# Optimization experiments

Hardware: AMD Instinct MI355X
Metric: run time of the kernel (lower is better)

The kernel has to match this reference:

```python
import jax, jax.numpy as jnp
import numpy as np

D_MODEL = 1024
N_HEAD = 16
D_HEAD = 64


def setup_inputs() -> dict:
    key = jax.random.key(0)
    k1, k2, k3 = jax.random.split(key, 3)
    B, T = 2, 2048
    x = jax.random.normal(k1, (B, T, D_MODEL), dtype=jnp.float32)
    # Linear weights (scaled like typical init to keep softmax numerics sane)
    w_attn = jax.random.normal(k2, (D_MODEL, 3 * D_MODEL), dtype=jnp.float32) * (1.0 / np.sqrt(D_MODEL))
    w_proj = jax.random.normal(k3, (D_MODEL, D_MODEL), dtype=jnp.float32) * (1.0 / np.sqrt(D_MODEL))
    return {"x": x, "w_attn": w_attn, "w_proj": w_proj}


def reference(x, w_attn, w_proj):
    B, T, C = x.shape
    # c_attn: fused qkv projection (use_bias=False)
    qkv = jnp.einsum('btc,cf->btf', x, w_attn)  # [B, T, 3C]
    q, k, v = jnp.split(qkv, 3, axis=-1)
    q = q.reshape(B, T, N_HEAD, D_HEAD)
    k = k.reshape(B, T, N_HEAD, D_HEAD)
    v = v.reshape(B, T, N_HEAD, D_HEAD)
    # scaled QK^T with causal mask (cache=None training path)
    att = jnp.einsum('bqhd,bkhd->bhqk', q, k) * (1.0 / jnp.sqrt(jnp.float32(D_HEAD)))
    causal = jnp.tril(jnp.ones((T, T), dtype=bool))  # [T, T]
    att = jnp.where(causal[None, None, :, :], att, -jnp.inf)
    att = jax.nn.softmax(att, axis=-1)
    # dropout is a no-op (deterministic / p=0)
    y = jnp.einsum('bhqk,bkhd->bqhd', att, v).reshape(B, T, C)
    y = jnp.einsum('btc,cd->btd', y, w_proj)
    return y
```

## Files before the change

### kernel.cpp

```cpp
#include <hip/hip_runtime.h>
#include <hip/hip_bf16.h>


typedef __attribute__((ext_vector_type(8))) __bf16 bf16x8;
typedef __attribute__((ext_vector_type(4))) float  floatx4;
typedef __attribute__((ext_vector_type(4))) float  fvec4;
typedef __attribute__((ext_vector_type(4))) short  short4v;

#define MFMA16(a, b, c) __builtin_amdgcn_mfma_f32_16x16x32_bf16(a, b, c, 0, 0, 0)

using as1v = const __attribute__((address_space(1))) void;
using as3v = __attribute__((address_space(3))) void;
__device__ __forceinline__ void async16(const void* g, void* l) {
  __builtin_amdgcn_global_load_lds((as1v*)g, (as3v*)l, 16, 0, 0);
}

__device__ inline void store_out(float* p, float v) { *p = v; }
__device__ inline void store_out(__hip_bfloat16* p, float v) { *p = __float2bfloat16(v); }

__global__ __launch_bounds__(256) void prep_kernel(const float* __restrict__ x,
                                                   const float* __restrict__ w_attn,
                                                   const float* __restrict__ w_proj,
                                                   __hip_bfloat16* __restrict__ xb,
                                                   __hip_bfloat16* __restrict__ wat,
                                                   __hip_bfloat16* __restrict__ wpt) {
  const int bid = blockIdx.x, tid = threadIdx.x;
  if (bid < 4096) {
    const int i = (bid * 256 + tid) * 4;
    fvec4 v = *(const fvec4*)(x + i);
    union { short4v s; __hip_bfloat16 h[4]; } u;
#pragma unroll
    for (int j = 0; j < 4; ++j) u.h[j] = __float2bfloat16(v[j]);
    *(short4v*)((short*)xb + i) = u.s;
    return;
  }
  __shared__ __align__(16) __hip_bfloat16 tile[64 * 64];
  const float* in;
  __hip_bfloat16* out;
  int cols, bx, by;
  if (bid < 4864) {
    const int b2 = bid - 4096;
    in = w_attn; out = wat; cols = 3072; bx = b2 % 48; by = b2 / 48;
  } else {
    const int b2 = bid - 4864;
    in = w_proj; out = wpt; cols = 1024; bx = b2 % 16; by = b2 / 16;
  }
  const int c0 = bx * 64, r0 = by * 64;
#pragma unroll
  for (int it = 0; it < 2; ++it) {
    const int c = it * 256 + tid;
    const int row = c >> 3, cg = c & 7;
    const float* src = in + (long)(r0 + row) * cols + c0 + cg * 8;
    fvec4 v0 = *(const fvec4*)src;
    fvec4 v1 = *(const fvec4*)(src + 4);
    union { bf16x8 v; __hip_bfloat16 h[8]; } u;
#pragma unroll
    for (int j = 0; j < 4; ++j) { u.h[j] = __float2bfloat16(v0[j]); u.h[4 + j] = __float2bfloat16(v1[j]); }
    *(bf16x8*)(tile + row * 64 + (cg ^ ((row >> 3) & 7)) * 8) = u.v;
  }
  __syncthreads();
#pragma unroll
  for (int it = 0; it < 2; ++it) {
    const int c = it * 256 + tid;
    const int dr = c >> 3, tg = c & 7;
    union { bf16x8 v; __hip_bfloat16 e[8]; } u;
    const int pg = (dr >> 3) ^ tg;
#pragma unroll
    for (int j = 0; j < 8; ++j)
      u.e[j] = tile[(tg * 8 + j) * 64 + pg * 8 + (dr & 7)];
    *(bf16x8*)(out + (long)(c0 + dr) * 1024 + r0 + tg * 8) = u.v;
  }
}

__global__ __launch_bounds__(256) void gemm_qkv_kernel(const __hip_bfloat16* __restrict__ A,
                                                       const __hip_bfloat16* __restrict__ Bt,
                                                       __hip_bfloat16* __restrict__ qk,
                                                       __hip_bfloat16* __restrict__ vt,
                                                       float qscale) {
  const int K = 1024;
  __shared__ __align__(16) __hip_bfloat16 As[2][128 * 32];
  __shared__ __align__(16) __hip_bfloat16 Bs[2][128 * 32];
  const int tid = threadIdx.x;
  const int lane = tid & 63, wv = tid >> 6;
  const int l15 = lane & 15, quad = lane >> 4;
  const int wm = wv >> 1, wn = wv & 1;
  const long m0 = (long)blockIdx.y * 128, n0 = (long)blockIdx.x * 128;
  floatx4 acc[4][4] = {};
  const int nk = K >> 5;

  auto issue = [&](int kt, int p) {
    const int k0 = kt << 5;
#pragma unroll
    for (int it = 0; it < 2; ++it) {
      const int c = it * 256 + tid;
      const int row = c >> 2;
      const int lcg = (c & 3) ^ ((row >> 1) & 3);
      async16(A + (m0 + row) * K + k0 + lcg * 8, (char*)&As[p][0] + c * 16);
      async16(Bt + (n0 + row) * K + k0 + lcg * 8, (char*)&Bs[p][0] + c * 16);
    }
  };

  issue(0, 0);
  for (int kt = 0; kt < nk; ++kt) {
    const int p = kt & 1;
    __syncthreads();
    if (kt + 1 < nk) issue(kt + 1, p ^ 1);
    bf16x8 af[4], bfr[4];
#pragma unroll
    for (int t = 0; t < 4; ++t) {
      const int ar = wm * 64 + t * 16 + l15;
      const int br = wn * 64 + t * 16 + l15;
      af[t]  = *(const bf16x8*)(&As[p][ar * 32 + (quad ^ ((ar >> 1) & 3)) * 8]);
      bfr[t] = *(const bf16x8*)(&Bs[p][br * 32 + (quad ^ ((br >> 1) & 3)) * 8]);
    }
#pragma unroll
    for (int mt = 0; mt < 4; ++mt)
#pragma unroll
      for (int nt = 0; nt < 4; ++nt)
        acc[mt][nt] = MFMA16(af[mt], bfr[nt], acc[mt][nt]);
  }

#pragma unroll
  for (int nt = 0; nt < 4; ++nt) {
    const int colb = (int)n0 + wn * 64 + nt * 16;
    if (colb >= 2048) {
      const int hh = (colb - 2048) >> 6;
      const int d  = (colb & 63) + l15;
#pragma unroll
      for (int mt = 0; mt < 4; ++mt) {
        const long row = m0 + wm * 64 + mt * 16 + quad * 4;
        const long b   = row >> 11;
        const long t0  = row & 2047;
        union { short4v s; __hip_bfloat16 h[4]; } uy;
#pragma unroll
        for (int r = 0; r < 4; ++r) uy.h[r] = __float2bfloat16(acc[mt][nt][r]);
        *(short4v*)(vt + ((b * 16 + hh) * 64 + d) * 2048 + t0) = uy.s;
      }
    } else {
      const float sc = (colb < 1024) ? qscale : 1.0f;
      const long col = colb + l15;
#pragma unroll
      for (int mt = 0; mt < 4; ++mt)
#pragma unroll
        for (int r = 0; r < 4; ++r) {
          const long row = m0 + wm * 64 + mt * 16 + quad * 4 + r;
          qk[row * 2048 + col] = __float2bfloat16(acc[mt][nt][r] * sc);
        }
    }
  }
}

template <typename OutT>
__global__ __launch_bounds__(256) void gemm_bt64_kernel(const __hip_bfloat16* __restrict__ A,
                                                        const __hip_bfloat16* __restrict__ Bt,
                                                        OutT* __restrict__ C,
                                                        int M, int N, int K) {
  __shared__ __align__(16) __hip_bfloat16 As[2][128 * 32];
  __shared__ __align__(16) __hip_bfloat16 Bs[2][64 * 32];
  const int tid = threadIdx.x;
  const int lane = tid & 63, wv = tid >> 6;
  const int l15 = lane & 15, quad = lane >> 4;
  const int wm = wv >> 1, wn = wv & 1;
  const long m0 = (long)blockIdx.y * 128, n0 = (long)blockIdx.x * 64;
  floatx4 acc[4][2] = {};
  const int nk = K >> 5;

  auto issue = [&](int kt, int p) {
    const int k0 = kt << 5;
#pragma unroll
    for (int it = 0; it < 2; ++it) {
      const int c = it * 256 + tid;
      const int row = c >> 2;
      const int lcg = (c & 3) ^ ((row >> 1) & 3);
      async16(A + (m0 + row) * K + k0 + lcg * 8, (char*)&As[p][0] + c * 16);
    }
    {
      const int c = tid;
      const int row = c >> 2;
      const int lcg = (c & 3) ^ ((row >> 1) & 3);
      async16(Bt + (n0 + row) * K + k0 + lcg * 8, (char*)&Bs[p][0] + c * 16);
    }
  };

  issue(0, 0);
  for (int kt = 0; kt < nk; ++kt) {
    const int p = kt & 1;
    __syncthreads();
    if (kt + 1 < nk) issue(kt + 1, p ^ 1);
    bf16x8 af[4], bfr[2];
#pragma unroll
    for (int t = 0; t < 4; ++t) {
      const int ar = wm * 64 + t * 16 + l15;
      af[t] = *(const bf16x8*)(&As[p][ar * 32 + (quad ^ ((ar >> 1) & 3)) * 8]);
    }
#pragma unroll
    for (int t = 0; t < 2; ++t) {
      const int br = wn * 32 + t * 16 + l15;
      bfr[t] = *(const bf16x8*)(&Bs[p][br * 32 + (quad ^ ((br >> 1) & 3)) * 8]);
    }
#pragma unroll
    for (int mt = 0; mt < 4; ++mt)
#pragma unroll
      for (int nt = 0; nt < 2; ++nt)
        acc[mt][nt] = MFMA16(af[mt], bfr[nt], acc[mt][nt]);
  }
#pragma unroll
  for (int mt = 0; mt < 4; ++mt)
#pragma unroll
    for (int nt = 0; nt < 2; ++nt)
#pragma unroll
      for (int r = 0; r < 4; ++r) {
        const long row = m0 + wm * 64 + mt * 16 + quad * 4 + r;
        const long col = n0 + wn * 32 + nt * 16 + l15;
        store_out(C + row * N + col, acc[mt][nt][r]);
      }
}

__global__ __launch_bounds__(256) void attn_kernel(const __hip_bfloat16* __restrict__ qk,
                                                   const __hip_bfloat16* __restrict__ vtg,
                                                   __hip_bfloat16* __restrict__ y) {
  __shared__ __align__(16) __hip_bfloat16 Ks[2][64 * 64];
  __shared__ __align__(16) __hip_bfloat16 Vt[2][64 * 64];
  __shared__ __align__(16) __hip_bfloat16 Pb[4][16 * 64];
  const int tid = threadIdx.x;
  const int lane = tid & 63, wv = tid >> 6;
  const int l15 = lane & 15, quad = lane >> 4;
  const int pt = blockIdx.x, h = blockIdx.y, b = blockIdx.z;
  const int qtA = pt, qtB = 31 - pt;
  const int q0A = qtA * 64, q0B = qtB * 64;
  const long bh = (long)b * 16 + h;
  const long RS = 2048;

  auto issue = [&](int kt, int p) {
    const int kb = kt * 64;
#pragma unroll
    for (int it = 0; it < 2; ++it) {
      const int c = it * 256 + tid;
      const int row = c >> 3;
      const int cg = (c & 7) ^ (row & 7);
      async16(qk + ((long)b * 2048 + kb + row) * RS + 1024 + h * 64 + cg * 8,
              (char*)&Ks[p][0] + c * 16);
      async16(vtg + (bh * 64 + row) * 2048 + kb + cg * 8, (char*)&Vt[p][0] + c * 16);
    }
  };

  bf16x8 bqA0, bqA1, bqB0, bqB1;
  {
    const __hip_bfloat16* qpA = qk + ((long)b * 2048 + q0A + wv * 16 + l15) * RS + h * 64 + quad * 8;
    bqA0 = *(const bf16x8*)qpA;
    bqA1 = *(const bf16x8*)(qpA + 32);
    const __hip_bfloat16* qpB = qk + ((long)b * 2048 + q0B + wv * 16 + l15) * RS + h * 64 + quad * 8;
    bqB0 = *(const bf16x8*)qpB;
    bqB1 = *(const bf16x8*)(qpB + 32);
  }
  union { bf16x8 v; __hip_bfloat16 e[8]; } uo;
#pragma unroll
  for (int j = 0; j < 8; ++j) uo.e[j] = __float2bfloat16(1.0f);
  const bf16x8 ones = uo.v;

  floatx4 oA[4] = {}, oB[4] = {}, o4A = {}, o4B = {};
  __hip_bfloat16* Pw = &Pb[wv][0];
  const int m7 = l15 & 7;

  issue(0, 0);
  for (int kt = 0; kt <= qtB; ++kt) {
    const int p = kt & 1;
    const int kb = kt * 64;
    const bool actA = (kt <= qtA);
    __syncthreads();
    if (kt < qtB) issue(kt + 1, p ^ 1);

    bf16x8 kf[4][2], vf[4][2];
#pragma unroll
    for (int nt = 0; nt < 4; ++nt) {
      const int row = nt * 16 + l15;
      const int s0 = (quad ^ (row & 7)) * 8, s1 = ((quad + 4) ^ (row & 7)) * 8;
      kf[nt][0] = *(const bf16x8*)(&Ks[p][row * 64 + s0]);
      kf[nt][1] = *(const bf16x8*)(&Ks[p][row * 64 + s1]);
      vf[nt][0] = *(const bf16x8*)(&Vt[p][row * 64 + s0]);
      vf[nt][1] = *(const bf16x8*)(&Vt[p][row * 64 + s1]);
    }

    auto tile = [&](const bf16x8& bq0, const bf16x8& bq1, floatx4* o, floatx4& o4,
                    bool diag, int q0X) {
      floatx4 st[4] = {};
#pragma unroll
      for (int nt = 0; nt < 4; ++nt) {
        st[nt] = MFMA16(kf[nt][0], bq0, st[nt]);
        st[nt] = MFMA16(kf[nt][1], bq1, st[nt]);
      }
      const int qg = q0X + wv * 16 + l15;
#pragma unroll
      for (int nt = 0; nt < 4; ++nt) {
        union { short4v s; __hip_bfloat16 h[4]; } up;
#pragma unroll
        for (int r = 0; r < 4; ++r) {
          float pv = exp2f(st[nt][r]);
          if (diag && (kb + nt * 16 + quad * 4 + r > qg)) pv = 0.f;
          up.h[r] = __float2bfloat16(pv);
        }
        const int chunk = (nt * 2 + (quad >> 1)) ^ m7;
        *(short4v*)(Pw + l15 * 64 + chunk * 8 + (quad & 1) * 4) = up.s;
      }
      const bf16x8 pb0 = *(const bf16x8*)(Pw + l15 * 64 + (quad ^ m7) * 8);
      const bf16x8 pb1 = *(const bf16x8*)(Pw + l15 * 64 + ((quad + 4) ^ m7) * 8);
#pragma unroll
      for (int mt = 0; mt < 4; ++mt) {
        o[mt] = MFMA16(vf[mt][0], pb0, o[mt]);
        o[mt] = MFMA16(vf[mt][1], pb1, o[mt]);
      }
      o4 = MFMA16(ones, pb0, o4);
      o4 = MFMA16(ones, pb1, o4);
    };

    tile(bqB0, bqB1, oB, o4B, kt == qtB, q0B);
    if (actA) tile(bqA0, bqA1, oA, o4A, kt == qtA, q0A);
  }

  auto epi = [&](floatx4* o, floatx4& o4, int q0X) {
    const float inv = 1.0f / o4[0];
    const long t = (long)b * 2048 + q0X + wv * 16 + l15;
#pragma unroll
    for (int mt = 0; mt < 4; ++mt) {
      union { short4v s; __hip_bfloat16 h[4]; } uy;
#pragma unroll
      for (int r = 0; r < 4; ++r) uy.h[r] = __float2bfloat16(o[mt][r] * inv);
      *(short4v*)(y + t * 1024 + h * 64 + mt * 16 + quad * 4) = uy.s;
    }
  };
  epi(oA, o4A, q0A);
  epi(oB, o4B, q0B);
}

extern "C" void kernel_launch(void* const* d_in, const int* in_sizes, int n_in,
                              void* d_out, int out_size, void* d_ws, size_t ws_size,
                              hipStream_t stream) {
  const float* x      = (const float*)d_in[0];
  const float* w_attn = (const float*)d_in[1];
  const float* w_proj = (const float*)d_in[2];
  float* out = (float*)d_out;
  char* ws = (char*)d_ws;
  __hip_bfloat16* xb  = (__hip_bfloat16*)(ws);
  __hip_bfloat16* wat = (__hip_bfloat16*)(ws + 8388608);
  __hip_bfloat16* qk  = (__hip_bfloat16*)(ws + 16777216);
  __hip_bfloat16* wpt = (__hip_bfloat16*)(ws + 33554432);
  __hip_bfloat16* vtg = (__hip_bfloat16*)(ws + 35651584);
  __hip_bfloat16* yb  = wat;
  const float SC = 0.18033688011112042f;

  prep_kernel<<<5120, 256, 0, stream>>>(x, w_attn, w_proj, xb, wat, wpt);
  gemm_qkv_kernel<<<dim3(24, 32), 256, 0, stream>>>(xb, wat, qk, vtg, SC);
  attn_kernel<<<dim3(16, 16, 2), 256, 0, stream>>>(qk, vtg, yb);
  gemm_bt64_kernel<float><<<dim3(16, 32), 256, 0, stream>>>(yb, wpt, out, 4096, 1024, 1024);
}
```

Measured before the change: 182.0 us.

## Stage V-transpose epilogue through LDS and interleave paired attention tiles

The QKV GEMM's V-transpose epilogue now writes the accumulator tile into the reused shared-memory buffer with a swizzle. It then emits full 16-byte coalesced stores to the transposed V layout, replacing scattered 8-byte stores. The attention kernel splits the P scratch into separate buffers for the two query tiles and interleaves their QK MFMAs, softmax and PV MFMAs. This exposes more independent MFMA work per iteration to hide latency, at the cost of more registers and doubled P shared memory.

```diff
diff --git a/kernel.cpp b/kernel.cpp
--- a/kernel.cpp
+++ b/kernel.cpp
@@ -78,8 +78,7 @@
                                                        __hip_bfloat16* __restrict__ vt,
                                                        float qscale) {
   const int K = 1024;
-  __shared__ __align__(16) __hip_bfloat16 As[2][128 * 32];
-  __shared__ __align__(16) __hip_bfloat16 Bs[2][128 * 32];
+  __shared__ __align__(16) __hip_bfloat16 smem[16384];
   const int tid = threadIdx.x;
   const int lane = tid & 63, wv = tid >> 6;
   const int l15 = lane & 15, quad = lane >> 4;
@@ -95,8 +94,8 @@
       const int c = it * 256 + tid;
       const int row = c >> 2;
       const int lcg = (c & 3) ^ ((row >> 1) & 3);
-      async16(A + (m0 + row) * K + k0 + lcg * 8, (char*)&As[p][0] + c * 16);
-      async16(Bt + (n0 + row) * K + k0 + lcg * 8, (char*)&Bs[p][0] + c * 16);
+      async16(A + (m0 + row) * K + k0 + lcg * 8, (char*)(smem + p * 4096) + c * 16);
+      async16(Bt + (n0 + row) * K + k0 + lcg * 8, (char*)(smem + 8192 + p * 4096) + c * 16);
     }
   };
 
@@ -105,13 +104,15 @@
     const int p = kt & 1;
     __syncthreads();
     if (kt + 1 < nk) issue(kt + 1, p ^ 1);
+    const __hip_bfloat16* As = smem + p * 4096;
+    const __hip_bfloat16* Bs = smem + 8192 + p * 4096;
     bf16x8 af[4], bfr[4];
 #pragma unroll
     for (int t = 0; t < 4; ++t) {
       const int ar = wm * 64 + t * 16 + l15;
       const int br = wn * 64 + t * 16 + l15;
-      af[t]  = *(const bf16x8*)(&As[p][ar * 32 + (quad ^ ((ar >> 1) & 3)) * 8]);
-      bfr[t] = *(const bf16x8*)(&Bs[p][br * 32 + (quad ^ ((br >> 1) & 3)) * 8]);
+      af[t]  = *(const bf16x8*)(As + ar * 32 + (quad ^ ((ar >> 1) & 3)) * 8);
+      bfr[t] = *(const bf16x8*)(Bs + br * 32 + (quad ^ ((br >> 1) & 3)) * 8);
     }
 #pragma unroll
     for (int mt = 0; mt < 4; ++mt)
@@ -120,23 +121,38 @@
         acc[mt][nt] = MFMA16(af[mt], bfr[nt], acc[mt][nt]);
   }
 
-#pragma unroll
-  for (int nt = 0; nt < 4; ++nt) {
-    const int colb = (int)n0 + wn * 64 + nt * 16;
-    if (colb >= 2048) {
-      const int hh = (colb - 2048) >> 6;
-      const int d  = (colb & 63) + l15;
-#pragma unroll
-      for (int mt = 0; mt < 4; ++mt) {
-        const long row = m0 + wm * 64 + mt * 16 + quad * 4;
-        const long b   = row >> 11;
-        const long t0  = row & 2047;
+  if (n0 >= 2048) {
+    __syncthreads();
+#pragma unroll
+    for (int mt = 0; mt < 4; ++mt)
+#pragma unroll
+      for (int nt = 0; nt < 4; ++nt) {
+        const int mb = wm * 64 + mt * 16 + quad * 4;
+        const int n  = wn * 64 + nt * 16 + l15;
+        const int cchunk = mb >> 4;
+        const int phys = cchunk ^ (n & 7);
         union { short4v s; __hip_bfloat16 h[4]; } uy;
 #pragma unroll
         for (int r = 0; r < 4; ++r) uy.h[r] = __float2bfloat16(acc[mt][nt][r]);
-        *(short4v*)(vt + ((b * 16 + hh) * 64 + d) * 2048 + t0) = uy.s;
-      }
-    } else {
+        *(short4v*)(smem + n * 128 + phys * 16 + (mb & 15)) = uy.s;
+      }
+    __syncthreads();
+    const int h0 = ((int)n0 - 2048) >> 6;
+    const long b  = m0 >> 11;
+    const long t0 = m0 & 2047;
+#pragma unroll
+    for (int j = 0; j < 8; ++j) {
+      const int idx = j * 256 + tid;
+      const int n = idx >> 4, lo = idx & 15;
+      const int phys = (lo >> 1) ^ (n & 7);
+      bf16x8 v = *(const bf16x8*)(smem + n * 128 + phys * 16 + (lo & 1) * 8);
+      const int h = h0 + (n >> 6), d = n & 63;
+      *(bf16x8*)(vt + ((b * 16 + h) * 64 + d) * 2048 + t0 + lo * 8) = v;
+    }
+  } else {
+#pragma unroll
+    for (int nt = 0; nt < 4; ++nt) {
+      const int colb = (int)n0 + wn * 64 + nt * 16;
       const float sc = (colb < 1024) ? qscale : 1.0f;
       const long col = colb + l15;
 #pragma unroll
@@ -221,7 +237,7 @@
                                                    __hip_bfloat16* __restrict__ y) {
   __shared__ __align__(16) __hip_bfloat16 Ks[2][64 * 64];
   __shared__ __align__(16) __hip_bfloat16 Vt[2][64 * 64];
-  __shared__ __align__(16) __hip_bfloat16 Pb[4][16 * 64];
+  __shared__ __align__(16) __hip_bfloat16 Pb[8192];
   const int tid = threadIdx.x;
   const int lane = tid & 63, wv = tid >> 6;
   const int l15 = lane & 15, quad = lane >> 4;
@@ -259,8 +275,10 @@
   const bf16x8 ones = uo.v;
 
   floatx4 oA[4] = {}, oB[4] = {}, o4A = {}, o4B = {};
-  __hip_bfloat16* Pw = &Pb[wv][0];
+  __hip_bfloat16* PwB = Pb + wv * 1024;
+  __hip_bfloat16* PwA = Pb + 4096 + wv * 1024;
   const int m7 = l15 & 7;
+  const int qg_off = wv * 16 + l15;
 
   issue(0, 0);
   for (int kt = 0; kt <= qtB; ++kt) {
@@ -281,40 +299,73 @@
       vf[nt][1] = *(const bf16x8*)(&Vt[p][row * 64 + s1]);
     }
 
-    auto tile = [&](const bf16x8& bq0, const bf16x8& bq1, floatx4* o, floatx4& o4,
-                    bool diag, int q0X) {
-      floatx4 st[4] = {};
+    floatx4 stB[4] = {}, stA[4] = {};
+#pragma unroll
+    for (int nt = 0; nt < 4; ++nt) {
+      stB[nt] = MFMA16(kf[nt][0], bqB0, stB[nt]);
+      stB[nt] = MFMA16(kf[nt][1], bqB1, stB[nt]);
+    }
+    if (actA) {
 #pragma unroll
       for (int nt = 0; nt < 4; ++nt) {
-        st[nt] = MFMA16(kf[nt][0], bq0, st[nt]);
-        st[nt] = MFMA16(kf[nt][1], bq1, st[nt]);
-      }
-      const int qg = q0X + wv * 16 + l15;
+        stA[nt] = MFMA16(kf[nt][0], bqA0, stA[nt]);
+        stA[nt] = MFMA16(kf[nt][1], bqA1, stA[nt]);
+      }
+    }
+
+    {
+      const int qg = q0B + qg_off;
+      const bool diag = (kt == qtB);
 #pragma unroll
       for (int nt = 0; nt < 4; ++nt) {
         union { short4v s; __hip_bfloat16 h[4]; } up;
 #pragma unroll
         for (int r = 0; r < 4; ++r) {
-          float pv = exp2f(st[nt][r]);
+          float pv = exp2f(stB[nt][r]);
           if (diag && (kb + nt * 16 + quad * 4 + r > qg)) pv = 0.f;
           up.h[r] = __float2bfloat16(pv);
         }
         const int chunk = (nt * 2 + (quad >> 1)) ^ m7;
-        *(short4v*)(Pw + l15 * 64 + chunk * 8 + (quad & 1) * 4) = up.s;
-      }
-      const bf16x8 pb0 = *(const bf16x8*)(Pw + l15 * 64 + (quad ^ m7) * 8);
-      const bf16x8 pb1 = *(const bf16x8*)(Pw + l15 * 64 + ((quad + 4) ^ m7) * 8);
+        *(short4v*)(PwB + l15 * 64 + chunk * 8 + (quad & 1) * 4) = up.s;
+      }
+    }
+    if (actA) {
+      const int qg = q0A + qg_off;
+      const bool diag = (kt == qtA);
+#pragma unroll
+      for (int nt = 0; nt < 4; ++nt) {
+        union { short4v s; __hip_bfloat16 h[4]; } up;
+#pragma unroll
+        for (int r = 0; r < 4; ++r) {
+          float pv = exp2f(stA[nt][r]);
+          if (diag && (kb + nt * 16 + quad * 4 + r > qg)) pv = 0.f;
+          up.h[r] = __float2bfloat16(pv);
+        }
+        const int chunk = (nt * 2 + (quad >> 1)) ^ m7;
+        *(short4v*)(PwA + l15 * 64 + chunk * 8 + (quad & 1) * 4) = up.s;
+      }
+    }
+
+    const bf16x8 pbB0 = *(const bf16x8*)(PwB + l15 * 64 + (quad ^ m7) * 8);
+    const bf16x8 pbB1 = *(const bf16x8*)(PwB + l15 * 64 + ((quad + 4) ^ m7) * 8);
+#pragma unroll
+    for (int mt = 0; mt < 4; ++mt) {
+      oB[mt] = MFMA16(vf[mt][0], pbB0, oB[mt]);
+      oB[mt] = MFMA16(vf[mt][1], pbB1, oB[mt]);
+    }
+    o4B = MFMA16(ones, pbB0, o4B);
+    o4B = MFMA16(ones, pbB1, o4B);
+    if (actA) {
+      const bf16x8 pbA0 = *(const bf16x8*)(PwA + l15 * 64 + (quad ^ m7) * 8);
+      const bf16x8 pbA1 = *(const bf16x8*)(PwA + l15 * 64 + ((quad + 4) ^ m7) * 8);
 #pragma unroll
       for (int mt = 0; mt < 4; ++mt) {
-        o[mt] = MFMA16(vf[mt][0], pb0, o[mt]);
-        o[mt] = MFMA16(vf[mt][1], pb1, o[mt]);
-      }
-      o4 = MFMA16(ones, pb0, o4);
-      o4 = MFMA16(ones, pb1, o4);
-    };
-
-    tile(bqB0, bqB1, oB, o4B, kt == qtB, q0B);
-    if (actA) tile(bqA0, bqA1, oA, o4A, kt == qtA, q0A);
+        oA[mt] = MFMA16(vf[mt][0], pbA0, oA[mt]);
+        oA[mt] = MFMA16(vf[mt][1], pbA1, oA[mt]);
+      }
+      o4A = MFMA16(ones, pbA0, o4A);
+      o4A = MFMA16(ones, pbA1, o4A);
+    }
   }
 
   auto epi = [&](floatx4* o, floatx4& o4, int q0X) {
```

New measurement: 187.1 us. 1.03x slower.

## Stage V-transpose epilogue through LDS, split P buffers, remap attention grid

Applied to the files above, without the earlier changes.

The QKV GEMM epilogue for V-columns now writes the accumulator tile into shared memory with a swizzle, then emits coalesced 16-byte stores to the transposed V layout instead of scattered 8-byte stores. The attention kernel gets separate P staging buffers for the A and B query tiles, which removes the write-after-read hazard between the two tile calls. It also uses a 1D grid remapped so that consecutive blocks share the same query-tile pair across heads, which may improve cache locality. The costs are an extra LDS round trip and two barriers in the epilogue, plus doubled P buffer LDS in attention.

```diff
diff --git a/kernel.cpp b/kernel.cpp
--- a/kernel.cpp
+++ b/kernel.cpp
@@ -78,8 +78,7 @@
                                                        __hip_bfloat16* __restrict__ vt,
                                                        float qscale) {
   const int K = 1024;
-  __shared__ __align__(16) __hip_bfloat16 As[2][128 * 32];
-  __shared__ __align__(16) __hip_bfloat16 Bs[2][128 * 32];
+  __shared__ __align__(16) __hip_bfloat16 smem[16384];
   const int tid = threadIdx.x;
   const int lane = tid & 63, wv = tid >> 6;
   const int l15 = lane & 15, quad = lane >> 4;
@@ -95,8 +94,8 @@
       const int c = it * 256 + tid;
       const int row = c >> 2;
       const int lcg = (c & 3) ^ ((row >> 1) & 3);
-      async16(A + (m0 + row) * K + k0 + lcg * 8, (char*)&As[p][0] + c * 16);
-      async16(Bt + (n0 + row) * K + k0 + lcg * 8, (char*)&Bs[p][0] + c * 16);
+      async16(A + (m0 + row) * K + k0 + lcg * 8, (char*)(smem + p * 4096) + c * 16);
+      async16(Bt + (n0 + row) * K + k0 + lcg * 8, (char*)(smem + 8192 + p * 4096) + c * 16);
     }
   };
 
@@ -105,13 +104,15 @@
     const int p = kt & 1;
     __syncthreads();
     if (kt + 1 < nk) issue(kt + 1, p ^ 1);
+    const __hip_bfloat16* As = smem + p * 4096;
+    const __hip_bfloat16* Bs = smem + 8192 + p * 4096;
     bf16x8 af[4], bfr[4];
 #pragma unroll
     for (int t = 0; t < 4; ++t) {
       const int ar = wm * 64 + t * 16 + l15;
       const int br = wn * 64 + t * 16 + l15;
-      af[t]  = *(const bf16x8*)(&As[p][ar * 32 + (quad ^ ((ar >> 1) & 3)) * 8]);
-      bfr[t] = *(const bf16x8*)(&Bs[p][br * 32 + (quad ^ ((br >> 1) & 3)) * 8]);
+      af[t]  = *(const bf16x8*)(As + ar * 32 + (quad ^ ((ar >> 1) & 3)) * 8);
+      bfr[t] = *(const bf16x8*)(Bs + br * 32 + (quad ^ ((br >> 1) & 3)) * 8);
     }
 #pragma unroll
     for (int mt = 0; mt < 4; ++mt)
@@ -120,23 +121,37 @@
         acc[mt][nt] = MFMA16(af[mt], bfr[nt], acc[mt][nt]);
   }
 
-#pragma unroll
-  for (int nt = 0; nt < 4; ++nt) {
-    const int colb = (int)n0 + wn * 64 + nt * 16;
-    if (colb >= 2048) {
-      const int hh = (colb - 2048) >> 6;
-      const int d  = (colb & 63) + l15;
-#pragma unroll
-      for (int mt = 0; mt < 4; ++mt) {
-        const long row = m0 + wm * 64 + mt * 16 + quad * 4;
-        const long b   = row >> 11;
-        const long t0  = row & 2047;
+  if (n0 >= 2048) {
+    __syncthreads();
+#pragma unroll
+    for (int mt = 0; mt < 4; ++mt)
+#pragma unroll
+      for (int nt = 0; nt < 4; ++nt) {
+        const int mb = wm * 64 + mt * 16 + quad * 4;
+        const int n  = wn * 64 + nt * 16 + l15;
+        const int phys = (mb >> 4) ^ (n & 7);
         union { short4v s; __hip_bfloat16 h[4]; } uy;
 #pragma unroll
         for (int r = 0; r < 4; ++r) uy.h[r] = __float2bfloat16(acc[mt][nt][r]);
-        *(short4v*)(vt + ((b * 16 + hh) * 64 + d) * 2048 + t0) = uy.s;
-      }
-    } else {
+        *(short4v*)(smem + n * 128 + phys * 16 + (mb & 15)) = uy.s;
+      }
+    __syncthreads();
+    const int h0 = ((int)n0 - 2048) >> 6;
+    const long b  = m0 >> 11;
+    const long t0 = m0 & 2047;
+#pragma unroll
+    for (int j = 0; j < 8; ++j) {
+      const int idx = j * 256 + tid;
+      const int n = idx >> 4, lo = idx & 15;
+      const int phys = (lo >> 1) ^ (n & 7);
+      bf16x8 v = *(const bf16x8*)(smem + n * 128 + phys * 16 + (lo & 1) * 8);
+      const int h = h0 + (n >> 6), d = n & 63;
+      *(bf16x8*)(vt + ((b * 16 + h) * 64 + d) * 2048 + t0 + lo * 8) = v;
+    }
+  } else {
+#pragma unroll
+    for (int nt = 0; nt < 4; ++nt) {
+      const int colb = (int)n0 + wn * 64 + nt * 16;
       const float sc = (colb < 1024) ? qscale : 1.0f;
       const long col = colb + l15;
 #pragma unroll
@@ -221,11 +236,14 @@
                                                    __hip_bfloat16* __restrict__ y) {
   __shared__ __align__(16) __hip_bfloat16 Ks[2][64 * 64];
   __shared__ __align__(16) __hip_bfloat16 Vt[2][64 * 64];
-  __shared__ __align__(16) __hip_bfloat16 Pb[4][16 * 64];
+  __shared__ __align__(16) __hip_bfloat16 Pb[8192];
   const int tid = threadIdx.x;
   const int lane = tid & 63, wv = tid >> 6;
   const int l15 = lane & 15, quad = lane >> 4;
-  const int pt = blockIdx.x, h = blockIdx.y, b = blockIdx.z;
+  const int bid = blockIdx.x;
+  const int pt = (bid >> 3) & 15;
+  const int hb = (bid >> 7) * 8 + (bid & 7);
+  const int h = hb & 15, b = hb >> 4;
   const int qtA = pt, qtB = 31 - pt;
   const int q0A = qtA * 64, q0B = qtB * 64;
   const long bh = (long)b * 16 + h;
@@ -259,7 +277,8 @@
   const bf16x8 ones = uo.v;
 
   floatx4 oA[4] = {}, oB[4] = {}, o4A = {}, o4B = {};
-  __hip_bfloat16* Pw = &Pb[wv][0];
+  __hip_bfloat16* PwB = Pb + wv * 1024;
+  __hip_bfloat16* PwA = Pb + 4096 + wv * 1024;
   const int m7 = l15 & 7;
 
   issue(0, 0);
@@ -282,7 +301,7 @@
     }
 
     auto tile = [&](const bf16x8& bq0, const bf16x8& bq1, floatx4* o, floatx4& o4,
-                    bool diag, int q0X) {
+                    __hip_bfloat16* Pw, bool diag, int q0X) {
       floatx4 st[4] = {};
 #pragma unroll
       for (int nt = 0; nt < 4; ++nt) {
@@ -313,8 +332,8 @@
       o4 = MFMA16(ones, pb1, o4);
     };
 
-    tile(bqB0, bqB1, oB, o4B, kt == qtB, q0B);
-    if (actA) tile(bqA0, bqA1, oA, o4A, kt == qtA, q0A);
+    tile(bqB0, bqB1, oB, o4B, PwB, kt == qtB, q0B);
+    if (actA) tile(bqA0, bqA1, oA, o4A, PwA, kt == qtA, q0A);
   }
 
   auto epi = [&](floatx4* o, floatx4& o4, int q0X) {
@@ -350,6 +369,6 @@
 
   prep_kernel<<<5120, 256, 0, stream>>>(x, w_attn, w_proj, xb, wat, wpt);
   gemm_qkv_kernel<<<dim3(24, 32), 256, 0, stream>>>(xb, wat, qk, vtg, SC);
-  attn_kernel<<<dim3(16, 16, 2), 256, 0, stream>>>(qk, vtg, yb);
+  attn_kernel<<<512, 256, 0, stream>>>(qk, vtg, yb);
   gemm_bt64_kernel<float><<<dim3(16, 32), 256, 0, stream>>>(yb, wpt, out, 4096, 1024, 1024);
 }
```

Measured after the change: 184.5 us. No clear change (+1.4%).

## Transpose MFMA operands for vectorized epilogue stores, remap attention grid, split P buffers

Applied to the files above, without the earlier changes.

In the QK part of the QKV GEMM and in the output projection GEMM, the MFMA operand order is swapped so each lane holds four consecutive columns. This lets the epilogue write 8-byte bf16 or 16-byte float vectors instead of scalar strided stores, cutting store instruction count and improving coalescing. The attention kernel moves to a 1D grid whose block index maps so that eight heads share each pair index, which may improve CU/XCD placement and L2 locality. It also gives the A and B tiles separate P scratch buffers so the two tile computations do not serialize on shared LDS, at the cost of doubling that buffer.

```diff
diff --git a/kernel.cpp b/kernel.cpp
--- a/kernel.cpp
+++ b/kernel.cpp
@@ -14,9 +14,6 @@
 __device__ __forceinline__ void async16(const void* g, void* l) {
   __builtin_amdgcn_global_load_lds((as1v*)g, (as3v*)l, 16, 0, 0);
 }
-
-__device__ inline void store_out(float* p, float v) { *p = v; }
-__device__ inline void store_out(__hip_bfloat16* p, float v) { *p = __float2bfloat16(v); }
 
 __global__ __launch_bounds__(256) void prep_kernel(const float* __restrict__ x,
                                                    const float* __restrict__ w_attn,
@@ -87,6 +84,7 @@
   const long m0 = (long)blockIdx.y * 128, n0 = (long)blockIdx.x * 128;
   floatx4 acc[4][4] = {};
   const int nk = K >> 5;
+  const bool isV = (n0 >= 2048);
 
   auto issue = [&](int kt, int p) {
     const int k0 = kt << 5;
@@ -113,17 +111,25 @@
       af[t]  = *(const bf16x8*)(&As[p][ar * 32 + (quad ^ ((ar >> 1) & 3)) * 8]);
       bfr[t] = *(const bf16x8*)(&Bs[p][br * 32 + (quad ^ ((br >> 1) & 3)) * 8]);
     }
-#pragma unroll
-    for (int mt = 0; mt < 4; ++mt)
-#pragma unroll
-      for (int nt = 0; nt < 4; ++nt)
-        acc[mt][nt] = MFMA16(af[mt], bfr[nt], acc[mt][nt]);
-  }
-
-#pragma unroll
-  for (int nt = 0; nt < 4; ++nt) {
-    const int colb = (int)n0 + wn * 64 + nt * 16;
-    if (colb >= 2048) {
+    if (isV) {
+#pragma unroll
+      for (int mt = 0; mt < 4; ++mt)
+#pragma unroll
+        for (int nt = 0; nt < 4; ++nt)
+          acc[mt][nt] = MFMA16(af[mt], bfr[nt], acc[mt][nt]);
+    } else {
+#pragma unroll
+      for (int mt = 0; mt < 4; ++mt)
+#pragma unroll
+        for (int nt = 0; nt < 4; ++nt)
+          acc[mt][nt] = MFMA16(bfr[nt], af[mt], acc[mt][nt]);
+    }
+  }
+
+  if (isV) {
+#pragma unroll
+    for (int nt = 0; nt < 4; ++nt) {
+      const int colb = (int)n0 + wn * 64 + nt * 16;
       const int hh = (colb - 2048) >> 6;
       const int d  = (colb & 63) + l15;
 #pragma unroll
@@ -136,24 +142,27 @@
         for (int r = 0; r < 4; ++r) uy.h[r] = __float2bfloat16(acc[mt][nt][r]);
         *(short4v*)(vt + ((b * 16 + hh) * 64 + d) * 2048 + t0) = uy.s;
       }
-    } else {
-      const float sc = (colb < 1024) ? qscale : 1.0f;
-      const long col = colb + l15;
-#pragma unroll
-      for (int mt = 0; mt < 4; ++mt)
-#pragma unroll
-        for (int r = 0; r < 4; ++r) {
-          const long row = m0 + wm * 64 + mt * 16 + quad * 4 + r;
-          qk[row * 2048 + col] = __float2bfloat16(acc[mt][nt][r] * sc);
-        }
-    }
-  }
-}
-
-template <typename OutT>
+    }
+  } else {
+#pragma unroll
+    for (int mt = 0; mt < 4; ++mt) {
+      const long row = m0 + wm * 64 + mt * 16 + l15;
+#pragma unroll
+      for (int nt = 0; nt < 4; ++nt) {
+        const int coln = (int)n0 + wn * 64 + nt * 16 + quad * 4;
+        const float sc = (coln < 1024) ? qscale : 1.0f;
+        union { short4v s; __hip_bfloat16 h[4]; } uy;
+#pragma unroll
+        for (int r = 0; r < 4; ++r) uy.h[r] = __float2bfloat16(acc[mt][nt][r] * sc);
+        *(short4v*)(qk + row * 2048 + coln) = uy.s;
+      }
+    }
+  }
+}
+
 __global__ __launch_bounds__(256) void gemm_bt64_kernel(const __hip_bfloat16* __restrict__ A,
                                                         const __hip_bfloat16* __restrict__ Bt,
-                                                        OutT* __restrict__ C,
+                                                        float* __restrict__ C,
                                                         int M, int N, int K) {
   __shared__ __align__(16) __hip_bfloat16 As[2][128 * 32];
   __shared__ __align__(16) __hip_bfloat16 Bs[2][64 * 32];
@@ -202,18 +211,20 @@
     for (int mt = 0; mt < 4; ++mt)
 #pragma unroll
       for (int nt = 0; nt < 2; ++nt)
-        acc[mt][nt] = MFMA16(af[mt], bfr[nt], acc[mt][nt]);
-  }
-#pragma unroll
-  for (int mt = 0; mt < 4; ++mt)
-#pragma unroll
-    for (int nt = 0; nt < 2; ++nt)
-#pragma unroll
-      for (int r = 0; r < 4; ++r) {
-        const long row = m0 + wm * 64 + mt * 16 + quad * 4 + r;
-        const long col = n0 + wn * 32 + nt * 16 + l15;
-        store_out(C + row * N + col, acc[mt][nt][r]);
-      }
+        acc[mt][nt] = MFMA16(bfr[nt], af[mt], acc[mt][nt]);
+  }
+#pragma unroll
+  for (int mt = 0; mt < 4; ++mt) {
+    const long row = m0 + wm * 64 + mt * 16 + l15;
+#pragma unroll
+    for (int nt = 0; nt < 2; ++nt) {
+      const int coln = (int)n0 + wn * 32 + nt * 16 + quad * 4;
+      fvec4 v;
+#pragma unroll
+      for (int r = 0; r < 4; ++r) v[r] = acc[mt][nt][r];
+      *(fvec4*)(C + row * N + coln) = v;
+    }
+  }
 }
 
 __global__ __launch_bounds__(256) void attn_kernel(const __hip_bfloat16* __restrict__ qk,
@@ -221,11 +232,14 @@
                                                    __hip_bfloat16* __restrict__ y) {
   __shared__ __align__(16) __hip_bfloat16 Ks[2][64 * 64];
   __shared__ __align__(16) __hip_bfloat16 Vt[2][64 * 64];
-  __shared__ __align__(16) __hip_bfloat16 Pb[4][16 * 64];
+  __shared__ __align__(16) __hip_bfloat16 Pb[8192];
   const int tid = threadIdx.x;
   const int lane = tid & 63, wv = tid >> 6;
   const int l15 = lane & 15, quad = lane >> 4;
-  const int pt = blockIdx.x, h = blockIdx.y, b = blockIdx.z;
+  const int bid = blockIdx.x;
+  const int pt = (bid >> 3) & 15;
+  const int hb = (bid >> 7) * 8 + (bid & 7);
+  const int h = hb & 15, b = hb >> 4;
   const int qtA = pt, qtB = 31 - pt;
   const int q0A = qtA * 64, q0B = qtB * 64;
   const long bh = (long)b * 16 + h;
@@ -259,7 +273,8 @@
   const bf16x8 ones = uo.v;
 
   floatx4 oA[4] = {}, oB[4] = {}, o4A = {}, o4B = {};
-  __hip_bfloat16* Pw = &Pb[wv][0];
+  __hip_bfloat16* PwB = Pb + wv * 1024;
+  __hip_bfloat16* PwA = Pb + 4096 + wv * 1024;
   const int m7 = l15 & 7;
 
   issue(0, 0);
@@ -282,7 +297,7 @@
     }
 
     auto tile = [&](const bf16x8& bq0, const bf16x8& bq1, floatx4* o, floatx4& o4,
-                    bool diag, int q0X) {
+                    __hip_bfloat16* Pw, bool diag, int q0X) {
       floatx4 st[4] = {};
 #pragma unroll
       for (int nt = 0; nt < 4; ++nt) {
@@ -313,8 +328,8 @@
       o4 = MFMA16(ones, pb1, o4);
     };
 
-    tile(bqB0, bqB1, oB, o4B, kt == qtB, q0B);
-    if (actA) tile(bqA0, bqA1, oA, o4A, kt == qtA, q0A);
+    tile(bqB0, bqB1, oB, o4B, PwB, kt == qtB, q0B);
+    if (actA) tile(bqA0, bqA1, oA, o4A, PwA, kt == qtA, q0A);
   }
 
   auto epi = [&](floatx4* o, floatx4& o4, int q0X) {
@@ -350,6 +365,6 @@
 
   prep_kernel<<<5120, 256, 0, stream>>>(x, w_attn, w_proj, xb, wat, wpt);
   gemm_qkv_kernel<<<dim3(24, 32), 256, 0, stream>>>(xb, wat, qk, vtg, SC);
-  attn_kernel<<<dim3(16, 16, 2), 256, 0, stream>>>(qk, vtg, yb);
-  gemm_bt64_kernel<float><<<dim3(16, 32), 256, 0, stream>>>(yb, wpt, out, 4096, 1024, 1024);
-}
+  attn_kernel<<<512, 256, 0, stream>>>(qk, vtg, yb);
+  gemm_bt64_kernel<<<dim3(16, 32), 256, 0, stream>>>(yb, wpt, out, 4096, 1024, 1024);
+}
```

After: 201.2 us. 10.6% more time.
